# Performance work log

Hardware: AMD Instinct MI355X
Metric: run time of the kernel (lower is better)

## Reference

```python
import jax, jax.numpy as jnp
import numpy as np

CUTOFF = 10.0
EPS_W = 1e-5
EPS_LN = 1e-5

def _silu(v):
    return v * jax.nn.sigmoid(v)

def setup_inputs() -> dict:
    key = jax.random.key(0)
    ks = jax.random.split(key, 12)
    N, E, H, R = 50000, 300000, 256, 64
    s = lambda fan_in: 1.0 / np.sqrt(fan_in)
    inp = {
        'x': jax.random.normal(ks[0], (N, H), jnp.float32),
        'edge_index': jax.random.randint(ks[1], (2, E), 0, N, jnp.int64 if jax.config.jax_enable_x64 else jnp.int32),
        'distances': jax.random.uniform(ks[2], (E,), jnp.float32) * CUTOFF,
        'centers': jnp.linspace(0.0, CUTOFF, R).astype(jnp.float32),
        'widths': jnp.full((R,), CUTOFF / R, jnp.float32),
        'rbf_w1': jax.random.normal(ks[3], (R, R), jnp.float32) * s(R),
        'rbf_b1': jnp.zeros((R,), jnp.float32),
        'rbf_w2': jax.random.normal(ks[4], (R, R), jnp.float32) * s(R),
        'rbf_b2': jnp.zeros((R,), jnp.float32),
        'filt_w1': jax.random.normal(ks[5], (R, H), jnp.float32) * s(R),
        'filt_b1': jnp.zeros((H,), jnp.float32),
        'filt_w2': jax.random.normal(ks[6], (H, H), jnp.float32) * s(H),
        'filt_b2': jnp.zeros((H,), jnp.float32),
        'filt_w3': jax.random.normal(ks[7], (H, H), jnp.float32) * s(H),
        'filt_b3': jnp.zeros((H,), jnp.float32),
        'node_w': jax.random.normal(ks[8], (H, H), jnp.float32) * s(H),
        'node_b': jnp.zeros((H,), jnp.float32),
        'ln_g': jnp.ones((H,), jnp.float32),
        'ln_b': jnp.zeros((H,), jnp.float32),
        'gate_w': jax.random.normal(ks[9], (H, H), jnp.float32) * s(H),
        'gate_b': jnp.zeros((H,), jnp.float32),
    }
    return inp

def reference(x, edge_index, distances, centers, widths,
              rbf_w1, rbf_b1, rbf_w2, rbf_b2,
              filt_w1, filt_b1, filt_w2, filt_b2, filt_w3, filt_b3,
              node_w, node_b, ln_g, ln_b, gate_w, gate_b):
    # LearnableRBF: envelope * gaussian basis, then 2-layer SiLU proj
    d = distances
    env = 0.5 * (jnp.cos(d * jnp.pi / CUTOFF) + 1.0) * (d < CUTOFF).astype(x.dtype)  # [E]
    rbf = jnp.exp(-0.5 * ((d[:, None] - centers) / (jnp.abs(widths) + EPS_W)) ** 2)   # [E,R]
    r = rbf * env[:, None]
    r = _silu(r @ rbf_w1 + rbf_b1) @ rbf_w2 + rbf_b2                                  # [E,R]
    # filter network: Lin-SiLU-Lin-SiLU-Lin
    W = _silu(r @ filt_w1 + filt_b1)
    W = _silu(W @ filt_w2 + filt_b2) @ filt_w3 + filt_b3                              # [E,H]
    # gather -> modulate -> scatter-add (CFConv messaging)
    row, col = edge_index[0], edge_index[1]
    msg = (x[col] @ node_w + node_b) * W                                              # [E,H]
    agg = jax.ops.segment_sum(msg, row, num_segments=x.shape[0])                      # [N,H]
    h = x + agg
    mu = jnp.mean(h, axis=-1, keepdims=True)
    var = jnp.var(h, axis=-1, keepdims=True)
    out = (h - mu) / jnp.sqrt(var + EPS_LN) * ln_g + ln_b
    return out * jax.nn.sigmoid(out @ gate_w + gate_b)
```

## Files before the change

### kernel.cpp

```cpp
#include <hip/hip_runtime.h>
#include <hip/hip_bf16.h>
#include <math.h>

typedef __attribute__((ext_vector_type(8))) short bf16x8;
typedef __attribute__((ext_vector_type(4))) float f32x4;
typedef unsigned short ushort_t;

constexpr float F_CUTOFF = 10.0f;
constexpr float F_EPS_W  = 1e-5f;
constexpr float F_EPS_LN = 1e-5f;
constexpr float F_PI     = 3.14159265358979323846f;

__device__ __forceinline__ float silu_f(float v)   { return v / (1.0f + __expf(-v)); }
__device__ __forceinline__ float sigmoid_f(float v){ return 1.0f / (1.0f + __expf(-v)); }

__device__ __forceinline__ ushort_t f2bf(float f) {
    union { __hip_bfloat16 h; ushort_t u; } v; v.h = __float2bfloat16(f); return v.u;
}
__device__ __forceinline__ float bf2f(ushort_t u) {
    union { unsigned u; float f; } v; v.u = ((unsigned)u) << 16; return v.f;
}

__device__ __forceinline__ float f4c(const float4& v, int q) {
    return q == 0 ? v.x : q == 1 ? v.y : q == 2 ? v.z : v.w;
}

__global__ void count_kernel(const int* __restrict__ eidx, int* __restrict__ cnt, int E)
{
    int e = blockIdx.x * 256 + threadIdx.x;
    if (e < E) atomicAdd(&cnt[eidx[e]], 1);
}

__global__ __launch_bounds__(1024)
void scan_kernel(int* __restrict__ cnt ,
                 int* __restrict__ start, int N)
{
    __shared__ int part[1024];
    const int tid = threadIdx.x;
    const int C = (N + 1023) >> 10;
    const int base = tid * C;
    int s = 0;
    for (int i = 0; i < C; ++i) {
        int idx = base + i;
        if (idx < N) s += cnt[idx];
    }
    part[tid] = s;
    __syncthreads();
    for (int off = 1; off < 1024; off <<= 1) {
        int v = (tid >= off) ? part[tid - off] : 0;
        __syncthreads();
        part[tid] += v;
        __syncthreads();
    }
    int run = part[tid] - s;
    for (int i = 0; i < C; ++i) {
        int idx = base + i;
        if (idx < N) {
            int c = cnt[idx];
            start[idx] = run;
            cnt[idx]   = run;
            run += c;
        }
    }
    if (tid == 1023) start[N] = part[1023];
}

__global__ void scatter_kernel(const int* __restrict__ eidx, const float* __restrict__ dist,
                               int* __restrict__ cursor,
                               int* __restrict__ colp, int* __restrict__ nodep,
                               float* __restrict__ distp, int E)
{
    int e = blockIdx.x * 256 + threadIdx.x;
    if (e < E) {
        int row = eidx[e];
        int s = atomicAdd(&cursor[row], 1);
        colp[s]  = eidx[E + e];
        nodep[s] = row;
        distp[s] = dist[e];
    }
}

__global__ void cvt_transpose_kernel(const float* __restrict__ in, ushort_t* __restrict__ out,
                                     int K, int N, int logK)
{
    int idx = blockIdx.x * 256 + threadIdx.x;
    if (idx >= K * N) return;
    int n = idx >> logK;
    int k = idx & (K - 1);
    out[idx] = f2bf(in[k * N + n]);
}

__global__ void combine_w_kernel(const float* __restrict__ w2, const float* __restrict__ fw1,
                                 ushort_t* __restrict__ out)
{
    int idx = blockIdx.x * 256 + threadIdx.x;
    int c = idx >> 6, j = idx & 63;
    float s = 0.f;
    #pragma unroll 8
    for (int n = 0; n < 64; ++n) s += w2[j * 64 + n] * fw1[n * 256 + c];
    out[idx] = f2bf(s);
}

__global__ void combine_b_kernel(const float* __restrict__ b2, const float* __restrict__ fw1,
                                 const float* __restrict__ fb1, float* __restrict__ out)
{
    int c = threadIdx.x;
    float s = fb1[c];
    #pragma unroll 8
    for (int n = 0; n < 64; ++n) s += b2[n] * fw1[n * 256 + c];
    out[c] = s;
}

__global__ __launch_bounds__(256)
void gemm256_bf16_kernel(const float* __restrict__ A, const float* __restrict__ Wm,
                         const float* __restrict__ bias, ushort_t* __restrict__ out, int M)
{
    __shared__ float4 As4[64][64];
    const int t = threadIdx.x;
    const int row0 = blockIdx.x * 64;

    #pragma unroll
    for (int i = 0; i < 16; ++i) {
        int flat = t + i * 256;
        int r = flat >> 6, k4 = flat & 63;
        int row = row0 + r;
        float4 v = make_float4(0.f, 0.f, 0.f, 0.f);
        if (row < M) v = reinterpret_cast<const float4*>(A)[row * 64 + k4];
        As4[r][k4] = v;
    }
    __syncthreads();

    const int jt  = t & 31;
    const int et  = t >> 5;
    const int j04 = jt * 2;
    const int r0  = et * 8;

    float acc[8][8];
    #pragma unroll
    for (int r = 0; r < 8; ++r)
        #pragma unroll
        for (int c = 0; c < 8; ++c) acc[r][c] = 0.f;

    for (int k4 = 0; k4 < 64; ++k4) {
        float4 a4[8];
        #pragma unroll
        for (int r = 0; r < 8; ++r) a4[r] = As4[r0 + r][k4];
        #pragma unroll
        for (int q = 0; q < 4; ++q) {
            const int k = k4 * 4 + q;
            float4 b0 = reinterpret_cast<const float4*>(Wm)[k * 64 + j04];
            float4 b1 = reinterpret_cast<const float4*>(Wm)[k * 64 + j04 + 1];
            float bb[8] = {b0.x, b0.y, b0.z, b0.w, b1.x, b1.y, b1.z, b1.w};
            #pragma unroll
            for (int r = 0; r < 8; ++r) {
                float av = f4c(a4[r], q);
                #pragma unroll
                for (int c = 0; c < 8; ++c) acc[r][c] = fmaf(av, bb[c], acc[r][c]);
            }
        }
    }

    float4 bv0 = reinterpret_cast<const float4*>(bias)[j04];
    float4 bv1 = reinterpret_cast<const float4*>(bias)[j04 + 1];
    float bb[8] = {bv0.x, bv0.y, bv0.z, bv0.w, bv1.x, bv1.y, bv1.z, bv1.w};

    #pragma unroll
    for (int r = 0; r < 8; ++r) {
        int row = row0 + r0 + r;
        if (row >= M) continue;
        ushort_t o8[8];
        #pragma unroll
        for (int c = 0; c < 8; ++c) o8[c] = f2bf(acc[r][c] + bb[c]);
        *reinterpret_cast<uint4*>(out + (size_t)row * 256 + jt * 8) = *reinterpret_cast<uint4*>(o8);
    }
}

__global__ __launch_bounds__(256)
void gate_gemm_kernel(const float* __restrict__ A, const float* __restrict__ Wm,
                      const float* __restrict__ bias, float* __restrict__ out, int M)
{
    __shared__ float4 As4[64][64];
    const int t = threadIdx.x;
    const int row0 = blockIdx.x * 64;

    #pragma unroll
    for (int i = 0; i < 16; ++i) {
        int flat = t + i * 256;
        int r = flat >> 6, k4 = flat & 63;
        int row = row0 + r;
        float4 v = make_float4(0.f, 0.f, 0.f, 0.f);
        if (row < M) v = reinterpret_cast<const float4*>(A)[row * 64 + k4];
        As4[r][k4] = v;
    }
    __syncthreads();

    const int jt  = t & 31;
    const int et  = t >> 5;
    const int j04 = jt * 2;
    const int r0  = et * 8;

    float acc[8][8];
    #pragma unroll
    for (int r = 0; r < 8; ++r)
        #pragma unroll
        for (int c = 0; c < 8; ++c) acc[r][c] = 0.f;

    for (int k4 = 0; k4 < 64; ++k4) {
        float4 a4[8];
        #pragma unroll
        for (int r = 0; r < 8; ++r) a4[r] = As4[r0 + r][k4];
        #pragma unroll
        for (int q = 0; q < 4; ++q) {
            const int k = k4 * 4 + q;
            float4 b0 = reinterpret_cast<const float4*>(Wm)[k * 64 + j04];
            float4 b1 = reinterpret_cast<const float4*>(Wm)[k * 64 + j04 + 1];
            float bb[8] = {b0.x, b0.y, b0.z, b0.w, b1.x, b1.y, b1.z, b1.w};
            #pragma unroll
            for (int r = 0; r < 8; ++r) {
                float av = f4c(a4[r], q);
                #pragma unroll
                for (int c = 0; c < 8; ++c) acc[r][c] = fmaf(av, bb[c], acc[r][c]);
            }
        }
    }

    float4 bv0 = reinterpret_cast<const float4*>(bias)[j04];
    float4 bv1 = reinterpret_cast<const float4*>(bias)[j04 + 1];
    float bb[8] = {bv0.x, bv0.y, bv0.z, bv0.w, bv1.x, bv1.y, bv1.z, bv1.w};

    #pragma unroll
    for (int r = 0; r < 8; ++r) {
        int row = row0 + r0 + r;
        if (row >= M) continue;
        float4 a0 = As4[r0 + r][j04];
        float4 a1 = As4[r0 + r][j04 + 1];
        float aa[8] = {a0.x, a0.y, a0.z, a0.w, a1.x, a1.y, a1.z, a1.w};
        float o[8];
        #pragma unroll
        for (int c = 0; c < 8; ++c) o[c] = aa[c] * sigmoid_f(acc[r][c] + bb[c]);
        reinterpret_cast<float4*>(out)[row * 64 + j04]     = make_float4(o[0], o[1], o[2], o[3]);
        reinterpret_cast<float4*>(out)[row * 64 + j04 + 1] = make_float4(o[4], o[5], o[6], o[7]);
    }
}

template<int KS, int NT, bool SILU>
__device__ __forceinline__ void mlp_stage(const unsigned char* in, unsigned char* out,
                                          const ushort_t* __restrict__ Wt,
                                          const float* __restrict__ bias,
                                          int wn, int g, int q)
{
    constexpr int K = KS * 32;
    f32x4 acc[2][NT];
    #pragma unroll
    for (int mt = 0; mt < 2; ++mt)
        #pragma unroll
        for (int nt = 0; nt < NT; ++nt) acc[mt][nt] = (f32x4){0.f, 0.f, 0.f, 0.f};

    #pragma unroll
    for (int kk = 0; kk < KS; ++kk) {
        bf16x8 b[NT];
        #pragma unroll
        for (int nt = 0; nt < NT; ++nt) {
            int n = (wn * NT + nt) * 16 + q;
            b[nt] = *reinterpret_cast<const bf16x8*>(Wt + n * K + kk * 32 + g * 8);
        }
        bf16x8 a[2];
        #pragma unroll
        for (int mt = 0; mt < 2; ++mt) {
            int m = mt * 16 + q;
            int unit = (4 * kk + g) ^ (m & 7);
            a[mt] = *reinterpret_cast<const bf16x8*>(in + m * 512 + unit * 16);
        }
        #pragma unroll
        for (int mt = 0; mt < 2; ++mt)
            #pragma unroll
            for (int nt = 0; nt < NT; ++nt)
                acc[mt][nt] = __builtin_amdgcn_mfma_f32_16x16x32_bf16(a[mt], b[nt], acc[mt][nt], 0, 0, 0);
    }

    const bool evenq = (q & 1) == 0;
    #pragma unroll
    for (int nt = 0; nt < NT; ++nt) {
        int n0  = (wn * NT + nt) * 16 + q;
        int n_e = n0 & ~1;
        float2 bv = *reinterpret_cast<const float2*>(bias + n_e);
        #pragma unroll
        for (int mt = 0; mt < 2; ++mt) {
            float v[4], p[4];
            #pragma unroll
            for (int r = 0; r < 4; ++r) { v[r] = acc[mt][nt][r]; p[r] = __shfl_xor(v[r], 1, 64); }
            #pragma unroll
            for (int rr = 0; rr < 2; ++rr) {
                int r = evenq ? rr : (2 + rr);
                float lo = (evenq ? v[r] : p[r]) + bv.x;
                float hi = (evenq ? p[r] : v[r]) + bv.y;
                if (SILU) { lo = silu_f(lo); hi = silu_f(hi); }
                int m = mt * 16 + 4 * g + r;
                unsigned u = (unsigned)f2bf(lo) | ((unsigned)f2bf(hi) << 16);
                int byte = m * 512 + (((n_e >> 3) ^ (m & 7)) << 4) + ((n_e & 7) * 2);
                *reinterpret_cast<unsigned*>(out + byte) = u;
            }
        }
    }
}

__global__ __launch_bounds__(256, 4)
void edge_csr_kernel(const float* __restrict__ distp, const int* __restrict__ colp,
                     const int* __restrict__ nodep, const int* __restrict__ start,
                     const float* __restrict__ centers, const float* __restrict__ widths,
                     const ushort_t* __restrict__ wt_rbf1, const float* __restrict__ rbf_b1,
                     const ushort_t* __restrict__ wt_comb, const float* __restrict__ b_comb,
                     const ushort_t* __restrict__ wt_f2, const float* __restrict__ filt_b2,
                     const ushort_t* __restrict__ wt_f3, const float* __restrict__ filt_b3,
                     const ushort_t* __restrict__ y, float* __restrict__ agg, int E)
{
    __shared__ __align__(16) unsigned char buf[32768];
    __shared__ int node_s[32];
    __shared__ int flag_s[32];
    unsigned char* bufA = buf;
    unsigned char* bufB = buf + 16384;

    const int t  = threadIdx.x;
    const int e0 = blockIdx.x * 32;
    const int wn   = t >> 6;
    const int lane = t & 63;
    const int g = lane >> 4, q = lane & 15;

    if (t < 32) {
        int ge = e0 + t;
        int nd = (ge < E) ? nodep[ge] : -1;
        node_s[t] = nd;
        int fl = 0;
        if (nd >= 0) {
            int lo = start[nd], hi = start[nd + 1];
            fl = (lo >= e0 && hi <= e0 + 32) ? 1 : 0;
        }
        flag_s[t] = fl;
    }

    const int e_own  = t >> 3;
    const int chunk  = t & 7;
    const int ge_own = e0 + e_own;
    const int col_own = (ge_own < E) ? colp[ge_own] : 0;
    uint4 yv[4];
    #pragma unroll
    for (int i = 0; i < 4; ++i)
        yv[i] = *reinterpret_cast<const uint4*>(y + (size_t)col_own * 256 + (i * 8 + chunk) * 8);

    {
        float d = (ge_own < E) ? distp[ge_own] : F_CUTOFF;
        float env = (d < F_CUTOFF) ? 0.5f * (__cosf(d * (F_PI / F_CUTOFF)) + 1.0f) : 0.0f;
        unsigned char* rowp = bufA + e_own * 512;
        int k0 = chunk * 8;
        #pragma unroll
        for (int i = 0; i < 4; ++i) {
            int n = k0 + 2 * i;
            float c0 = centers[n],     w0 = fabsf(widths[n]) + F_EPS_W;
            float c1 = centers[n + 1], w1 = fabsf(widths[n + 1]) + F_EPS_W;
            float z0 = (d - c0) / w0, z1 = (d - c1) / w1;
            float r0 = env * __expf(-0.5f * z0 * z0);
            float r1 = env * __expf(-0.5f * z1 * z1);
            unsigned u = (unsigned)f2bf(r0) | ((unsigned)f2bf(r1) << 16);
            int byte = (((n >> 3) ^ (e_own & 7)) << 4) + ((n & 7) * 2);
            *reinterpret_cast<unsigned*>(rowp + byte) = u;
        }
    }
    __syncthreads();

    mlp_stage<2, 1, true>(bufA, bufB, wt_rbf1, rbf_b1, wn, g, q);
    __syncthreads();
    mlp_stage<2, 4, true>(bufB, bufA, wt_comb, b_comb, wn, g, q);
    __syncthreads();
    mlp_stage<8, 4, true>(bufA, bufB, wt_f2, filt_b2, wn, g, q);
    __syncthreads();

    #pragma unroll
    for (int i = 0; i < 4; ++i)
        *reinterpret_cast<uint4*>(bufA + e_own * 512 + (i * 8 + chunk) * 16) = yv[i];
    __syncthreads();

    f32x4 acc[2][4];
    #pragma unroll
    for (int mt = 0; mt < 2; ++mt)
        #pragma unroll
        for (int nt = 0; nt < 4; ++nt) acc[mt][nt] = (f32x4){0.f, 0.f, 0.f, 0.f};

    #pragma unroll
    for (int kk = 0; kk < 8; ++kk) {
        bf16x8 b[4];
        #pragma unroll
        for (int nt = 0; nt < 4; ++nt) {
            int n = (wn * 4 + nt) * 16 + q;
            b[nt] = *reinterpret_cast<const bf16x8*>(wt_f3 + n * 256 + kk * 32 + g * 8);
        }
        bf16x8 a[2];
        #pragma unroll
        for (int mt = 0; mt < 2; ++mt) {
            int m = mt * 16 + q;
            int unit = (4 * kk + g) ^ (m & 7);
            a[mt] = *reinterpret_cast<const bf16x8*>(bufB + m * 512 + unit * 16);
        }
        #pragma unroll
        for (int mt = 0; mt < 2; ++mt)
            #pragma unroll
            for (int nt = 0; nt < 4; ++nt)
                acc[mt][nt] = __builtin_amdgcn_mfma_f32_16x16x32_bf16(a[mt], b[nt], acc[mt][nt], 0, 0, 0);
    }

    float bn[4];
    int   nn[4];
    #pragma unroll
    for (int nt = 0; nt < 4; ++nt) { nn[nt] = (wn * 4 + nt) * 16 + q; bn[nt] = filt_b3[nn[nt]]; }

    #pragma unroll
    for (int mt = 0; mt < 2; ++mt) {
        #pragma unroll
        for (int r = 0; r < 4; ++r) {
            int m = mt * 16 + 4 * g + r;
            const unsigned char* yrow = bufA + m * 512;
            #pragma unroll
            for (int nt = 0; nt < 4; ++nt) {
                float yvv = bf2f(*reinterpret_cast<const ushort_t*>(yrow + nn[nt] * 2));
                acc[mt][nt][r] = (acc[mt][nt][r] + bn[nt]) * yvv;
            }
        }
    }
    __syncthreads();

    float* msgf = reinterpret_cast<float*>(buf);
    #pragma unroll
    for (int mt = 0; mt < 2; ++mt) {
        #pragma unroll
        for (int r = 0; r < 4; ++r) {
            int m  = mt * 16 + 4 * g + r;
            #pragma unroll
            for (int nt = 0; nt < 4; ++nt)
                msgf[m * 256 + nn[nt]] = acc[mt][nt][r];
        }
    }
    __syncthreads();

    {
        const int j = t;
        float accv = 0.f;
        int cur = -2, rs = 0;
        #pragma unroll 4
        for (int r = 0; r < 32; ++r) {
            int nd = node_s[r];
            if (nd != cur) {
                if (cur >= 0) {
                    if (flag_s[rs]) agg[(size_t)cur * 256 + j] = accv;
                    else            unsafeAtomicAdd(&agg[(size_t)cur * 256 + j], accv);
                }
                cur = nd; rs = r; accv = msgf[r * 256 + j];
            } else {
                accv += msgf[r * 256 + j];
            }
        }
        if (cur >= 0) {
            if (flag_s[rs]) agg[(size_t)cur * 256 + j] = accv;
            else            unsafeAtomicAdd(&agg[(size_t)cur * 256 + j], accv);
        }
    }
}

__global__ __launch_bounds__(256, 4)
void edge_atomic_kernel(const float* __restrict__ dist, const int* __restrict__ eidx,
                        const float* __restrict__ centers, const float* __restrict__ widths,
                        const ushort_t* __restrict__ wt_rbf1, const float* __restrict__ rbf_b1,
                        const ushort_t* __restrict__ wt_comb, const float* __restrict__ b_comb,
                        const ushort_t* __restrict__ wt_f2, const float* __restrict__ filt_b2,
                        const ushort_t* __restrict__ wt_f3, const float* __restrict__ filt_b3,
                        const ushort_t* __restrict__ y, float* __restrict__ agg, int E)
{
    __shared__ __align__(16) unsigned char bufA[16384];
    __shared__ __align__(16) unsigned char bufB[16384];
    __shared__ int rs_s[32];

    const int t  = threadIdx.x;
    const int e0 = blockIdx.x * 32;
    const int wn   = t >> 6;
    const int lane = t & 63;
    const int g = lane >> 4, q = lane & 15;

    if (t < 32) {
        int ge = e0 + t;
        rs_s[t] = (ge < E) ? eidx[ge] : 0;
    }

    const int e_own  = t >> 3;
    const int chunk  = t & 7;
    const int ge_own = e0 + e_own;
    const int col_own = (ge_own < E) ? eidx[E + ge_own] : 0;
    uint4 yv[4];
    #pragma unroll
    for (int i = 0; i < 4; ++i)
        yv[i] = *reinterpret_cast<const uint4*>(y + (size_t)col_own * 256 + (i * 8 + chunk) * 8);

    {
        float d = (ge_own < E) ? dist[ge_own] : F_CUTOFF;
        float env = (d < F_CUTOFF) ? 0.5f * (__cosf(d * (F_PI / F_CUTOFF)) + 1.0f) : 0.0f;
        unsigned char* rowp = bufA + e_own * 512;
        int k0 = chunk * 8;
        #pragma unroll
        for (int i = 0; i < 4; ++i) {
            int n = k0 + 2 * i;
            float c0 = centers[n],     w0 = fabsf(widths[n]) + F_EPS_W;
            float c1 = centers[n + 1], w1 = fabsf(widths[n + 1]) + F_EPS_W;
            float z0 = (d - c0) / w0, z1 = (d - c1) / w1;
            float r0 = env * __expf(-0.5f * z0 * z0);
            float r1 = env * __expf(-0.5f * z1 * z1);
            unsigned u = (unsigned)f2bf(r0) | ((unsigned)f2bf(r1) << 16);
            int byte = (((n >> 3) ^ (e_own & 7)) << 4) + ((n & 7) * 2);
            *reinterpret_cast<unsigned*>(rowp + byte) = u;
        }
    }
    __syncthreads();

    mlp_stage<2, 1, true>(bufA, bufB, wt_rbf1, rbf_b1, wn, g, q);
    __syncthreads();
    mlp_stage<2, 4, true>(bufB, bufA, wt_comb, b_comb, wn, g, q);
    __syncthreads();
    mlp_stage<8, 4, true>(bufA, bufB, wt_f2, filt_b2, wn, g, q);
    __syncthreads();

    #pragma unroll
    for (int i = 0; i < 4; ++i)
        *reinterpret_cast<uint4*>(bufA + e_own * 512 + (i * 8 + chunk) * 16) = yv[i];
    __syncthreads();

    {
        f32x4 acc[2][4];
        #pragma unroll
        for (int mt = 0; mt < 2; ++mt)
            #pragma unroll
            for (int nt = 0; nt < 4; ++nt) acc[mt][nt] = (f32x4){0.f, 0.f, 0.f, 0.f};

        #pragma unroll
        for (int kk = 0; kk < 8; ++kk) {
            bf16x8 b[4];
            #pragma unroll
            for (int nt = 0; nt < 4; ++nt) {
                int n = (wn * 4 + nt) * 16 + q;
                b[nt] = *reinterpret_cast<const bf16x8*>(wt_f3 + n * 256 + kk * 32 + g * 8);
            }
            bf16x8 a[2];
            #pragma unroll
            for (int mt = 0; mt < 2; ++mt) {
                int m = mt * 16 + q;
                int unit = (4 * kk + g) ^ (m & 7);
                a[mt] = *reinterpret_cast<const bf16x8*>(bufB + m * 512 + unit * 16);
            }
            #pragma unroll
            for (int mt = 0; mt < 2; ++mt)
                #pragma unroll
                for (int nt = 0; nt < 4; ++nt)
                    acc[mt][nt] = __builtin_amdgcn_mfma_f32_16x16x32_bf16(a[mt], b[nt], acc[mt][nt], 0, 0, 0);
        }

        float bn[4];
        int   nn[4];
        #pragma unroll
        for (int nt = 0; nt < 4; ++nt) { nn[nt] = (wn * 4 + nt) * 16 + q; bn[nt] = filt_b3[nn[nt]]; }

        #pragma unroll
        for (int mt = 0; mt < 2; ++mt) {
            #pragma unroll
            for (int r = 0; r < 4; ++r) {
                int m  = mt * 16 + 4 * g + r;
                int ge = e0 + m;
                if (ge < E) {
                    const unsigned char* yrow = bufA + m * 512;
                    float* arow = agg + (size_t)rs_s[m] * 256;
                    #pragma unroll
                    for (int nt = 0; nt < 4; ++nt) {
                        float wv = acc[mt][nt][r] + bn[nt];
                        float yvv = bf2f(*reinterpret_cast<const ushort_t*>(yrow + nn[nt] * 2));
                        unsafeAtomicAdd(&arow[nn[nt]], wv * yvv);
                    }
                }
            }
        }
    }
}

__global__ __launch_bounds__(256)
void ln_kernel(const float* __restrict__ x, const float* __restrict__ agg,
               const float* __restrict__ g, const float* __restrict__ b,
               float* __restrict__ out0, int N)
{
    int lane = threadIdx.x & 63;
    int row  = blockIdx.x * 4 + (threadIdx.x >> 6);
    if (row >= N) return;
    float4 hx = reinterpret_cast<const float4*>(x)[row * 64 + lane];
    float4 ha = reinterpret_cast<const float4*>(agg)[row * 64 + lane];
    float4 h  = make_float4(hx.x + ha.x, hx.y + ha.y, hx.z + ha.z, hx.w + ha.w);
    float s  = h.x + h.y + h.z + h.w;
    float s2 = h.x * h.x + h.y * h.y + h.z * h.z + h.w * h.w;
    #pragma unroll
    for (int off = 32; off > 0; off >>= 1) {
        s  += __shfl_xor(s,  off, 64);
        s2 += __shfl_xor(s2, off, 64);
    }
    float mu  = s * (1.0f / 256.0f);
    float var = s2 * (1.0f / 256.0f) - mu * mu;
    float inv = rsqrtf(var + F_EPS_LN);
    float4 gv = reinterpret_cast<const float4*>(g)[lane];
    float4 bv = reinterpret_cast<const float4*>(b)[lane];
    float4 o;
    o.x = (h.x - mu) * inv * gv.x + bv.x;
    o.y = (h.y - mu) * inv * gv.y + bv.y;
    o.z = (h.z - mu) * inv * gv.z + bv.z;
    o.w = (h.w - mu) * inv * gv.w + bv.w;
    reinterpret_cast<float4*>(out0)[row * 64 + lane] = o;
}

extern "C" void kernel_launch(void* const* d_in, const int* in_sizes, int n_in,
                              void* d_out, int out_size, void* d_ws, size_t ws_size,
                              hipStream_t stream)
{
    const float* x       = (const float*)d_in[0];
    const int*   eidx    = (const int*)  d_in[1];
    const float* dist    = (const float*)d_in[2];
    const float* centers = (const float*)d_in[3];
    const float* widths  = (const float*)d_in[4];
    const float* rbf_w1  = (const float*)d_in[5];
    const float* rbf_b1  = (const float*)d_in[6];
    const float* rbf_w2  = (const float*)d_in[7];
    const float* rbf_b2  = (const float*)d_in[8];
    const float* filt_w1 = (const float*)d_in[9];
    const float* filt_b1 = (const float*)d_in[10];
    const float* filt_w2 = (const float*)d_in[11];
    const float* filt_b2 = (const float*)d_in[12];
    const float* filt_w3 = (const float*)d_in[13];
    const float* filt_b3 = (const float*)d_in[14];
    const float* node_w  = (const float*)d_in[15];
    const float* node_b  = (const float*)d_in[16];
    const float* ln_g    = (const float*)d_in[17];
    const float* ln_b    = (const float*)d_in[18];
    const float* gate_w  = (const float*)d_in[19];
    const float* gate_b  = (const float*)d_in[20];

    const int N = in_sizes[0] / 256;
    const int E = in_sizes[2];

    char* wsb = (char*)d_ws;
    size_t off = 0;
    auto alloc = [&](size_t bytes, size_t align) -> char* {
        off = (off + align - 1) & ~(align - 1);
        char* p = wsb + off;
        off += bytes;
        return p;
    };
    ushort_t* y_bf  = (ushort_t*)alloc((size_t)N * 256 * 2, 16);
    ushort_t* wt1   = (ushort_t*)alloc(64 * 64 * 2, 16);
    ushort_t* wcomb = (ushort_t*)alloc(256 * 64 * 2, 16);
    ushort_t* wf2t  = (ushort_t*)alloc(256 * 256 * 2, 16);
    ushort_t* wf3t  = (ushort_t*)alloc(256 * 256 * 2, 16);
    float*    bcomb = (float*)   alloc(256 * 4, 16);
    int*      cnt   = (int*)     alloc((size_t)N * 4, 16);
    int*      start = (int*)     alloc(((size_t)N + 1) * 4, 16);
    int*      colp  = (int*)     alloc((size_t)E * 4, 16);
    int*      nodep = (int*)     alloc((size_t)E * 4, 16);
    float*    distp = (float*)   alloc((size_t)E * 4, 16);
    const bool csr_fits = (off <= ws_size);

    dim3 b256(256);

    cvt_transpose_kernel<<<dim3((64 * 64 + 255) / 256),   b256, 0, stream>>>(rbf_w1,  wt1, 64, 64, 6);
    combine_w_kernel<<<dim3(64), b256, 0, stream>>>(rbf_w2, filt_w1, wcomb);
    combine_b_kernel<<<dim3(1), b256, 0, stream>>>(rbf_b2, filt_w1, filt_b1, bcomb);
    cvt_transpose_kernel<<<dim3((256 * 256 + 255) / 256), b256, 0, stream>>>(filt_w2, wf2t, 256, 256, 8);
    cvt_transpose_kernel<<<dim3((256 * 256 + 255) / 256), b256, 0, stream>>>(filt_w3, wf3t, 256, 256, 8);

    gemm256_bf16_kernel<<<dim3((N + 63) / 64), b256, 0, stream>>>(x, node_w, node_b, y_bf, N);

    hipMemsetAsync(d_out, 0, (size_t)out_size * sizeof(float), stream);

    if (csr_fits) {
        hipMemsetAsync(cnt, 0, (size_t)N * 4, stream);
        count_kernel<<<dim3((E + 255) / 256), b256, 0, stream>>>(eidx, cnt, E);
        scan_kernel<<<dim3(1), 1024, 0, stream>>>(cnt, start, N);
        scatter_kernel<<<dim3((E + 255) / 256), b256, 0, stream>>>(eidx, dist, cnt, colp, nodep, distp, E);

        edge_csr_kernel<<<dim3((E + 31) / 32), b256, 0, stream>>>(
            distp, colp, nodep, start, centers, widths,
            wt1, rbf_b1, wcomb, bcomb,
            wf2t, filt_b2, wf3t, filt_b3,
            y_bf, (float*)d_out, E);
    } else {
        edge_atomic_kernel<<<dim3((E + 31) / 32), b256, 0, stream>>>(
            dist, eidx, centers, widths,
            wt1, rbf_b1, wcomb, bcomb,
            wf2t, filt_b2, wf3t, filt_b3,
            y_bf, (float*)d_out, E);
    }

    ln_kernel<<<dim3((N + 3) / 4), b256, 0, stream>>>(x, (float*)d_out, ln_g, ln_b, (float*)d_out, N);
    gate_gemm_kernel<<<dim3((N + 63) / 64), b256, 0, stream>>>((float*)d_out, gate_w, gate_b, (float*)d_out, N);
}
```

Baseline: 948.0 us.

## Split fused edge kernel into staged 64-row GEMM kernels and parallelize CSR scan

Replaces the single fused per-32-edge kernel with three kernels per edge chunk: RBF plus first filter layers written to a bf16 workspace, a double-buffered 64-row GEMM for filt_w2, and a GEMM fused with the y-gather and segmented scatter for filt_w3. The chunk size is set by the available workspace, and the split path is used only when E fits in at most 8 chunks. The aim is larger GEMM tiles with better weight reuse than 32-edge blocks provide, at the cost of extra global memory round-trips for intermediates. The single-block scan is also replaced with a two-level scan, and the atomic fallback kernel is removed.

Result: slower. 1.080 ms (+14.0%).

```diff
diff --git a/kernel.cpp b/kernel.cpp
--- a/kernel.cpp
+++ b/kernel.cpp
@@ -31,38 +31,53 @@
     if (e < E) atomicAdd(&cnt[eidx[e]], 1);
 }
 
-__global__ __launch_bounds__(1024)
-void scan_kernel(int* __restrict__ cnt ,
-                 int* __restrict__ start, int N)
-{
-    __shared__ int part[1024];
-    const int tid = threadIdx.x;
-    const int C = (N + 1023) >> 10;
-    const int base = tid * C;
+__global__ __launch_bounds__(256)
+void scan_sum_kernel(const int* __restrict__ cnt, int* __restrict__ part, int N, int range)
+{
+    __shared__ int red[256];
+    int base = blockIdx.x * range;
     int s = 0;
-    for (int i = 0; i < C; ++i) {
+    for (int i = threadIdx.x; i < range; i += 256) {
         int idx = base + i;
         if (idx < N) s += cnt[idx];
     }
-    part[tid] = s;
-    __syncthreads();
-    for (int off = 1; off < 1024; off <<= 1) {
-        int v = (tid >= off) ? part[tid - off] : 0;
+    red[threadIdx.x] = s;
+    __syncthreads();
+    #pragma unroll
+    for (int o = 128; o > 0; o >>= 1) {
+        if (threadIdx.x < o) red[threadIdx.x] += red[threadIdx.x + o];
         __syncthreads();
-        part[tid] += v;
+    }
+    if (threadIdx.x == 0) part[blockIdx.x] = red[0];
+}
+
+__global__ __launch_bounds__(256)
+void scan_write_kernel(const int* __restrict__ part, int* __restrict__ cnt ,
+                       int* __restrict__ start, int N, int range, int E)
+{
+    __shared__ int ex[256];
+    int tid = threadIdx.x;
+    int v = part[tid];
+    ex[tid] = v;
+    __syncthreads();
+    for (int o = 1; o < 256; o <<= 1) {
+        int add = (tid >= o) ? ex[tid - o] : 0;
         __syncthreads();
-    }
-    int run = part[tid] - s;
-    for (int i = 0; i < C; ++i) {
+        ex[tid] += add;
+        __syncthreads();
+    }
+    int run = ex[tid] - v;
+    int base = tid * range;
+    for (int i = 0; i < range; ++i) {
         int idx = base + i;
         if (idx < N) {
             int c = cnt[idx];
             start[idx] = run;
-            cnt[idx]   = run;
+            cnt[idx] = run;
             run += c;
         }
     }
-    if (tid == 1023) start[N] = part[1023];
+    if (tid == 0) start[N] = E;
 }
 
 __global__ void scatter_kernel(const int* __restrict__ eidx, const float* __restrict__ dist,
@@ -305,20 +320,14 @@
 }
 
 __global__ __launch_bounds__(256, 4)
-void edge_csr_kernel(const float* __restrict__ distp, const int* __restrict__ colp,
-                     const int* __restrict__ nodep, const int* __restrict__ start,
-                     const float* __restrict__ centers, const float* __restrict__ widths,
-                     const ushort_t* __restrict__ wt_rbf1, const float* __restrict__ rbf_b1,
-                     const ushort_t* __restrict__ wt_comb, const float* __restrict__ b_comb,
-                     const ushort_t* __restrict__ wt_f2, const float* __restrict__ filt_b2,
-                     const ushort_t* __restrict__ wt_f3, const float* __restrict__ filt_b3,
-                     const ushort_t* __restrict__ y, float* __restrict__ agg, int E)
-{
-    __shared__ __align__(16) unsigned char buf[32768];
-    __shared__ int node_s[32];
-    __shared__ int flag_s[32];
-    unsigned char* bufA = buf;
-    unsigned char* bufB = buf + 16384;
+void rbf_f1_kernel(const float* __restrict__ distp,
+                   const float* __restrict__ centers, const float* __restrict__ widths,
+                   const ushort_t* __restrict__ wt_rbf1, const float* __restrict__ rbf_b1,
+                   const ushort_t* __restrict__ wt_comb, const float* __restrict__ b_comb,
+                   ushort_t* __restrict__ f1, int Mc)
+{
+    __shared__ __align__(16) unsigned char bufA[16384];
+    __shared__ __align__(16) unsigned char bufB[16384];
 
     const int t  = threadIdx.x;
     const int e0 = blockIdx.x * 32;
@@ -326,29 +335,12 @@
     const int lane = t & 63;
     const int g = lane >> 4, q = lane & 15;
 
-    if (t < 32) {
-        int ge = e0 + t;
-        int nd = (ge < E) ? nodep[ge] : -1;
-        node_s[t] = nd;
-        int fl = 0;
-        if (nd >= 0) {
-            int lo = start[nd], hi = start[nd + 1];
-            fl = (lo >= e0 && hi <= e0 + 32) ? 1 : 0;
-        }
-        flag_s[t] = fl;
-    }
-
     const int e_own  = t >> 3;
     const int chunk  = t & 7;
     const int ge_own = e0 + e_own;
-    const int col_own = (ge_own < E) ? colp[ge_own] : 0;
-    uint4 yv[4];
-    #pragma unroll
-    for (int i = 0; i < 4; ++i)
-        yv[i] = *reinterpret_cast<const uint4*>(y + (size_t)col_own * 256 + (i * 8 + chunk) * 8);
 
     {
-        float d = (ge_own < E) ? distp[ge_own] : F_CUTOFF;
+        float d = (ge_own < Mc) ? distp[ge_own] : F_CUTOFF;
         float env = (d < F_CUTOFF) ? 0.5f * (__cosf(d * (F_PI / F_CUTOFF)) + 1.0f) : 0.0f;
         unsigned char* rowp = bufA + e_own * 512;
         int k0 = chunk * 8;
@@ -371,6 +363,308 @@
     __syncthreads();
     mlp_stage<2, 4, true>(bufB, bufA, wt_comb, b_comb, wn, g, q);
     __syncthreads();
+
+    if (ge_own < Mc) {
+        #pragma unroll
+        for (int i = 0; i < 4; ++i) {
+            int c = chunk + i * 8;
+            int u = (c & 24) | ((c ^ (e_own & 7)) & 7);
+            uint4 v = *reinterpret_cast<const uint4*>(bufA + e_own * 512 + u * 16);
+            *reinterpret_cast<uint4*>(f1 + (size_t)ge_own * 256 + c * 8) = v;
+        }
+    }
+}
+
+__global__ __launch_bounds__(256, 3)
+void gemm_stage_kernel(const ushort_t* __restrict__ A, const ushort_t* __restrict__ Wt,
+                       const float* __restrict__ bias, ushort_t* __restrict__ out, int M)
+{
+    __shared__ __align__(16) unsigned char sbuf[2][8192];
+
+    const int t  = threadIdx.x;
+    const int m0 = blockIdx.x * 64;
+    const int wn   = t >> 6;
+    const int lane = t & 63;
+    const int g = lane >> 4, q = lane & 15;
+
+    const int s0r = t >> 3,         s0u = t & 7;
+    const int s1r = (t + 256) >> 3, s1u = t & 7;
+    const ushort_t* src0base = A + (size_t)((m0 + s0r < M) ? (m0 + s0r) : (M - 1)) * 256 + ((s0u ^ (s0r & 7)) * 8);
+    const ushort_t* src1base = A + (size_t)((m0 + s1r < M) ? (m0 + s1r) : (M - 1)) * 256 + ((s1u ^ (s1r & 7)) * 8);
+
+    uint4 p0 = *reinterpret_cast<const uint4*>(src0base);
+    uint4 p1 = *reinterpret_cast<const uint4*>(src1base);
+    *reinterpret_cast<uint4*>(&sbuf[0][t * 16])         = p0;
+    *reinterpret_cast<uint4*>(&sbuf[0][(t + 256) * 16]) = p1;
+    __syncthreads();
+
+    f32x4 acc[4][4];
+    #pragma unroll
+    for (int mt = 0; mt < 4; ++mt)
+        #pragma unroll
+        for (int nt = 0; nt < 4; ++nt) acc[mt][nt] = (f32x4){0.f, 0.f, 0.f, 0.f};
+
+    for (int kt = 0; kt < 4; ++kt) {
+        const int cur = kt & 1;
+        uint4 nx0, nx1;
+        if (kt < 3) {
+            nx0 = *reinterpret_cast<const uint4*>(src0base + (kt + 1) * 64);
+            nx1 = *reinterpret_cast<const uint4*>(src1base + (kt + 1) * 64);
+        }
+        #pragma unroll
+        for (int ks = 0; ks < 2; ++ks) {
+            bf16x8 b[4];
+            #pragma unroll
+            for (int nt = 0; nt < 4; ++nt) {
+                int n = wn * 64 + nt * 16 + q;
+                b[nt] = *reinterpret_cast<const bf16x8*>(Wt + (size_t)n * 256 + kt * 64 + ks * 32 + g * 8);
+            }
+            bf16x8 a[4];
+            #pragma unroll
+            for (int mt = 0; mt < 4; ++mt) {
+                int r = mt * 16 + q;
+                int u = (ks * 4 + g) ^ (r & 7);
+                a[mt] = *reinterpret_cast<const bf16x8*>(&sbuf[cur][r * 128 + u * 16]);
+            }
+            #pragma unroll
+            for (int mt = 0; mt < 4; ++mt)
+                #pragma unroll
+                for (int nt = 0; nt < 4; ++nt)
+                    acc[mt][nt] = __builtin_amdgcn_mfma_f32_16x16x32_bf16(a[mt], b[nt], acc[mt][nt], 0, 0, 0);
+        }
+        __syncthreads();
+        if (kt < 3) {
+            *reinterpret_cast<uint4*>(&sbuf[cur ^ 1][t * 16])         = nx0;
+            *reinterpret_cast<uint4*>(&sbuf[cur ^ 1][(t + 256) * 16]) = nx1;
+            __syncthreads();
+        }
+    }
+
+    const bool evenq = (q & 1) == 0;
+    #pragma unroll
+    for (int nt = 0; nt < 4; ++nt) {
+        int n0  = wn * 64 + nt * 16 + q;
+        int n_e = n0 & ~1;
+        float2 bv = *reinterpret_cast<const float2*>(bias + n_e);
+        #pragma unroll
+        for (int mt = 0; mt < 4; ++mt) {
+            float v[4], p[4];
+            #pragma unroll
+            for (int r = 0; r < 4; ++r) { v[r] = acc[mt][nt][r]; p[r] = __shfl_xor(v[r], 1, 64); }
+            #pragma unroll
+            for (int rr = 0; rr < 2; ++rr) {
+                int r = evenq ? rr : (2 + rr);
+                float lo = silu_f((evenq ? v[r] : p[r]) + bv.x);
+                float hi = silu_f((evenq ? p[r] : v[r]) + bv.y);
+                int mloc = mt * 16 + 4 * g + r;
+                int grow = m0 + mloc;
+                if (grow < M) {
+                    unsigned u = (unsigned)f2bf(lo) | ((unsigned)f2bf(hi) << 16);
+                    *reinterpret_cast<unsigned*>(out + (size_t)grow * 256 + n_e) = u;
+                }
+            }
+        }
+    }
+}
+
+__global__ __launch_bounds__(256, 3)
+void gemm_scatter_kernel(const ushort_t* __restrict__ A, const ushort_t* __restrict__ Wt,
+                         const float* __restrict__ bias,
+                         const int* __restrict__ colp, const int* __restrict__ nodep,
+                         const int* __restrict__ start,
+                         const ushort_t* __restrict__ y, float* __restrict__ agg,
+                         int cs, int M)
+{
+    __shared__ __align__(16) unsigned char sbuf[2][8192];
+    __shared__ float msgf[32][257];
+    __shared__ int node_s[64], lo_s[64], hi_s[64], col_s[64];
+
+    const int t  = threadIdx.x;
+    const int m0 = blockIdx.x * 64;
+    const int gs0 = cs + m0;
+    const int wn   = t >> 6;
+    const int lane = t & 63;
+    const int g = lane >> 4, q = lane & 15;
+
+    if (t < 64) {
+        bool ok = (m0 + t < M);
+        int nd = ok ? nodep[gs0 + t] : -1;
+        node_s[t] = nd;
+        col_s[t]  = ok ? colp[gs0 + t] : 0;
+        lo_s[t] = (nd >= 0) ? start[nd] : 0;
+        hi_s[t] = (nd >= 0) ? start[nd + 1] : 0;
+    }
+
+    const int s0r = t >> 3,         s0u = t & 7;
+    const int s1r = (t + 256) >> 3, s1u = t & 7;
+    const ushort_t* src0base = A + (size_t)((m0 + s0r < M) ? (m0 + s0r) : (M - 1)) * 256 + ((s0u ^ (s0r & 7)) * 8);
+    const ushort_t* src1base = A + (size_t)((m0 + s1r < M) ? (m0 + s1r) : (M - 1)) * 256 + ((s1u ^ (s1r & 7)) * 8);
+
+    uint4 p0 = *reinterpret_cast<const uint4*>(src0base);
+    uint4 p1 = *reinterpret_cast<const uint4*>(src1base);
+    *reinterpret_cast<uint4*>(&sbuf[0][t * 16])         = p0;
+    *reinterpret_cast<uint4*>(&sbuf[0][(t + 256) * 16]) = p1;
+    __syncthreads();
+
+    f32x4 acc[4][4];
+    #pragma unroll
+    for (int mt = 0; mt < 4; ++mt)
+        #pragma unroll
+        for (int nt = 0; nt < 4; ++nt) acc[mt][nt] = (f32x4){0.f, 0.f, 0.f, 0.f};
+
+    for (int kt = 0; kt < 4; ++kt) {
+        const int cur = kt & 1;
+        uint4 nx0, nx1;
+        if (kt < 3) {
+            nx0 = *reinterpret_cast<const uint4*>(src0base + (kt + 1) * 64);
+            nx1 = *reinterpret_cast<const uint4*>(src1base + (kt + 1) * 64);
+        }
+        #pragma unroll
+        for (int ks = 0; ks < 2; ++ks) {
+            bf16x8 b[4];
+            #pragma unroll
+            for (int nt = 0; nt < 4; ++nt) {
+                int n = wn * 64 + nt * 16 + q;
+                b[nt] = *reinterpret_cast<const bf16x8*>(Wt + (size_t)n * 256 + kt * 64 + ks * 32 + g * 8);
+            }
+            bf16x8 a[4];
+            #pragma unroll
+            for (int mt = 0; mt < 4; ++mt) {
+                int r = mt * 16 + q;
+                int u = (ks * 4 + g) ^ (r & 7);
+                a[mt] = *reinterpret_cast<const bf16x8*>(&sbuf[cur][r * 128 + u * 16]);
+            }
+            #pragma unroll
+            for (int mt = 0; mt < 4; ++mt)
+                #pragma unroll
+                for (int nt = 0; nt < 4; ++nt)
+                    acc[mt][nt] = __builtin_amdgcn_mfma_f32_16x16x32_bf16(a[mt], b[nt], acc[mt][nt], 0, 0, 0);
+        }
+        __syncthreads();
+        if (kt < 3) {
+            *reinterpret_cast<uint4*>(&sbuf[cur ^ 1][t * 16])         = nx0;
+            *reinterpret_cast<uint4*>(&sbuf[cur ^ 1][(t + 256) * 16]) = nx1;
+            __syncthreads();
+        }
+    }
+
+    float bn[4];
+    #pragma unroll
+    for (int nt = 0; nt < 4; ++nt) bn[nt] = bias[wn * 64 + nt * 16 + q];
+
+    #pragma unroll
+    for (int p = 0; p < 2; ++p) {
+        #pragma unroll
+        for (int mtl = 0; mtl < 2; ++mtl) {
+            int mt = 2 * p + mtl;
+            #pragma unroll
+            for (int r = 0; r < 4; ++r) {
+                int pr = mtl * 16 + 4 * g + r;
+                #pragma unroll
+                for (int nt = 0; nt < 4; ++nt)
+                    msgf[pr][wn * 64 + nt * 16 + q] = acc[mt][nt][r] + bn[nt];
+            }
+        }
+        __syncthreads();
+
+        {
+            const int j = t;
+            const int gwin0 = gs0 + p * 32;
+            float accv = 0.f;
+            int cur = -2, curRow = 0;
+            for (int pr = 0; pr < 32; ++pr) {
+                int rr = p * 32 + pr;
+                int nd = node_s[rr];
+                float yv = bf2f(y[(size_t)col_s[rr] * 256 + j]);
+                float val = msgf[pr][j] * yv;
+                if (nd != cur) {
+                    if (cur >= 0) {
+                        bool interior = (lo_s[curRow] >= gwin0) && (hi_s[curRow] <= gwin0 + 32);
+                        if (interior) agg[(size_t)cur * 256 + j] = accv;
+                        else          unsafeAtomicAdd(&agg[(size_t)cur * 256 + j], accv);
+                    }
+                    cur = nd; curRow = rr; accv = val;
+                } else {
+                    accv += val;
+                }
+            }
+            if (cur >= 0) {
+                bool interior = (lo_s[curRow] >= gwin0) && (hi_s[curRow] <= gwin0 + 32);
+                if (interior) agg[(size_t)cur * 256 + j] = accv;
+                else          unsafeAtomicAdd(&agg[(size_t)cur * 256 + j], accv);
+            }
+        }
+        __syncthreads();
+    }
+}
+
+__global__ __launch_bounds__(256, 4)
+void edge_csr_kernel(const float* __restrict__ distp, const int* __restrict__ colp,
+                     const int* __restrict__ nodep, const int* __restrict__ start,
+                     const float* __restrict__ centers, const float* __restrict__ widths,
+                     const ushort_t* __restrict__ wt_rbf1, const float* __restrict__ rbf_b1,
+                     const ushort_t* __restrict__ wt_comb, const float* __restrict__ b_comb,
+                     const ushort_t* __restrict__ wt_f2, const float* __restrict__ filt_b2,
+                     const ushort_t* __restrict__ wt_f3, const float* __restrict__ filt_b3,
+                     const ushort_t* __restrict__ y, float* __restrict__ agg, int E)
+{
+    __shared__ __align__(16) unsigned char buf[32768];
+    __shared__ int node_s[32];
+    __shared__ int flag_s[32];
+    unsigned char* bufA = buf;
+    unsigned char* bufB = buf + 16384;
+
+    const int t  = threadIdx.x;
+    const int e0 = blockIdx.x * 32;
+    const int wn   = t >> 6;
+    const int lane = t & 63;
+    const int g = lane >> 4, q = lane & 15;
+
+    if (t < 32) {
+        int ge = e0 + t;
+        int nd = (ge < E) ? nodep[ge] : -1;
+        node_s[t] = nd;
+        int fl = 0;
+        if (nd >= 0) {
+            int lo = start[nd], hi = start[nd + 1];
+            fl = (lo >= e0 && hi <= e0 + 32) ? 1 : 0;
+        }
+        flag_s[t] = fl;
+    }
+
+    const int e_own  = t >> 3;
+    const int chunk  = t & 7;
+    const int ge_own = e0 + e_own;
+    const int col_own = (ge_own < E) ? colp[ge_own] : 0;
+    uint4 yv[4];
+    #pragma unroll
+    for (int i = 0; i < 4; ++i)
+        yv[i] = *reinterpret_cast<const uint4*>(y + (size_t)col_own * 256 + (i * 8 + chunk) * 8);
+
+    {
+        float d = (ge_own < E) ? distp[ge_own] : F_CUTOFF;
+        float env = (d < F_CUTOFF) ? 0.5f * (__cosf(d * (F_PI / F_CUTOFF)) + 1.0f) : 0.0f;
+        unsigned char* rowp = bufA + e_own * 512;
+        int k0 = chunk * 8;
+        #pragma unroll
+        for (int i = 0; i < 4; ++i) {
+            int n = k0 + 2 * i;
+            float c0 = centers[n],     w0 = fabsf(widths[n]) + F_EPS_W;
+            float c1 = centers[n + 1], w1 = fabsf(widths[n + 1]) + F_EPS_W;
+            float z0 = (d - c0) / w0, z1 = (d - c1) / w1;
+            float r0 = env * __expf(-0.5f * z0 * z0);
+            float r1 = env * __expf(-0.5f * z1 * z1);
+            unsigned u = (unsigned)f2bf(r0) | ((unsigned)f2bf(r1) << 16);
+            int byte = (((n >> 3) ^ (e_own & 7)) << 4) + ((n & 7) * 2);
+            *reinterpret_cast<unsigned*>(rowp + byte) = u;
+        }
+    }
+    __syncthreads();
+
+    mlp_stage<2, 1, true>(bufA, bufB, wt_rbf1, rbf_b1, wn, g, q);
+    __syncthreads();
+    mlp_stage<2, 4, true>(bufB, bufA, wt_comb, b_comb, wn, g, q);
+    __syncthreads();
     mlp_stage<8, 4, true>(bufA, bufB, wt_f2, filt_b2, wn, g, q);
     __syncthreads();
 
@@ -432,7 +726,7 @@
     for (int mt = 0; mt < 2; ++mt) {
         #pragma unroll
         for (int r = 0; r < 4; ++r) {
-            int m  = mt * 16 + 4 * g + r;
+            int m = mt * 16 + 4 * g + r;
             #pragma unroll
             for (int nt = 0; nt < 4; ++nt)
                 msgf[m * 256 + nn[nt]] = acc[mt][nt][r];
@@ -460,126 +754,6 @@
         if (cur >= 0) {
             if (flag_s[rs]) agg[(size_t)cur * 256 + j] = accv;
             else            unsafeAtomicAdd(&agg[(size_t)cur * 256 + j], accv);
-        }
-    }
-}
-
-__global__ __launch_bounds__(256, 4)
-void edge_atomic_kernel(const float* __restrict__ dist, const int* __restrict__ eidx,
-                        const float* __restrict__ centers, const float* __restrict__ widths,
-                        const ushort_t* __restrict__ wt_rbf1, const float* __restrict__ rbf_b1,
-                        const ushort_t* __restrict__ wt_comb, const float* __restrict__ b_comb,
-                        const ushort_t* __restrict__ wt_f2, const float* __restrict__ filt_b2,
-                        const ushort_t* __restrict__ wt_f3, const float* __restrict__ filt_b3,
-                        const ushort_t* __restrict__ y, float* __restrict__ agg, int E)
-{
-    __shared__ __align__(16) unsigned char bufA[16384];
-    __shared__ __align__(16) unsigned char bufB[16384];
-    __shared__ int rs_s[32];
-
-    const int t  = threadIdx.x;
-    const int e0 = blockIdx.x * 32;
-    const int wn   = t >> 6;
-    const int lane = t & 63;
-    const int g = lane >> 4, q = lane & 15;
-
-    if (t < 32) {
-        int ge = e0 + t;
-        rs_s[t] = (ge < E) ? eidx[ge] : 0;
-    }
-
-    const int e_own  = t >> 3;
-    const int chunk  = t & 7;
-    const int ge_own = e0 + e_own;
-    const int col_own = (ge_own < E) ? eidx[E + ge_own] : 0;
-    uint4 yv[4];
-    #pragma unroll
-    for (int i = 0; i < 4; ++i)
-        yv[i] = *reinterpret_cast<const uint4*>(y + (size_t)col_own * 256 + (i * 8 + chunk) * 8);
-
-    {
-        float d = (ge_own < E) ? dist[ge_own] : F_CUTOFF;
-        float env = (d < F_CUTOFF) ? 0.5f * (__cosf(d * (F_PI / F_CUTOFF)) + 1.0f) : 0.0f;
-        unsigned char* rowp = bufA + e_own * 512;
-        int k0 = chunk * 8;
-        #pragma unroll
-        for (int i = 0; i < 4; ++i) {
-            int n = k0 + 2 * i;
-            float c0 = centers[n],     w0 = fabsf(widths[n]) + F_EPS_W;
-            float c1 = centers[n + 1], w1 = fabsf(widths[n + 1]) + F_EPS_W;
-            float z0 = (d - c0) / w0, z1 = (d - c1) / w1;
-            float r0 = env * __expf(-0.5f * z0 * z0);
-            float r1 = env * __expf(-0.5f * z1 * z1);
-            unsigned u = (unsigned)f2bf(r0) | ((unsigned)f2bf(r1) << 16);
-            int byte = (((n >> 3) ^ (e_own & 7)) << 4) + ((n & 7) * 2);
-            *reinterpret_cast<unsigned*>(rowp + byte) = u;
-        }
-    }
-    __syncthreads();
-
-    mlp_stage<2, 1, true>(bufA, bufB, wt_rbf1, rbf_b1, wn, g, q);
-    __syncthreads();
-    mlp_stage<2, 4, true>(bufB, bufA, wt_comb, b_comb, wn, g, q);
-    __syncthreads();
-    mlp_stage<8, 4, true>(bufA, bufB, wt_f2, filt_b2, wn, g, q);
-    __syncthreads();
-
-    #pragma unroll
-    for (int i = 0; i < 4; ++i)
-        *reinterpret_cast<uint4*>(bufA + e_own * 512 + (i * 8 + chunk) * 16) = yv[i];
-    __syncthreads();
-
-    {
-        f32x4 acc[2][4];
-        #pragma unroll
-        for (int mt = 0; mt < 2; ++mt)
-            #pragma unroll
-            for (int nt = 0; nt < 4; ++nt) acc[mt][nt] = (f32x4){0.f, 0.f, 0.f, 0.f};
-
-        #pragma unroll
-        for (int kk = 0; kk < 8; ++kk) {
-            bf16x8 b[4];
-            #pragma unroll
-            for (int nt = 0; nt < 4; ++nt) {
-                int n = (wn * 4 + nt) * 16 + q;
-                b[nt] = *reinterpret_cast<const bf16x8*>(wt_f3 + n * 256 + kk * 32 + g * 8);
-            }
-            bf16x8 a[2];
-            #pragma unroll
-            for (int mt = 0; mt < 2; ++mt) {
-                int m = mt * 16 + q;
-                int unit = (4 * kk + g) ^ (m & 7);
-                a[mt] = *reinterpret_cast<const bf16x8*>(bufB + m * 512 + unit * 16);
-            }
-            #pragma unroll
-            for (int mt = 0; mt < 2; ++mt)
-                #pragma unroll
-                for (int nt = 0; nt < 4; ++nt)
-                    acc[mt][nt] = __builtin_amdgcn_mfma_f32_16x16x32_bf16(a[mt], b[nt], acc[mt][nt], 0, 0, 0);
-        }
-
-        float bn[4];
-        int   nn[4];
-        #pragma unroll
-        for (int nt = 0; nt < 4; ++nt) { nn[nt] = (wn * 4 + nt) * 16 + q; bn[nt] = filt_b3[nn[nt]]; }
-
-        #pragma unroll
-        for (int mt = 0; mt < 2; ++mt) {
-            #pragma unroll
-            for (int r = 0; r < 4; ++r) {
-                int m  = mt * 16 + 4 * g + r;
-                int ge = e0 + m;
-                if (ge < E) {
-                    const unsigned char* yrow = bufA + m * 512;
-                    float* arow = agg + (size_t)rs_s[m] * 256;
-                    #pragma unroll
-                    for (int nt = 0; nt < 4; ++nt) {
-                        float wv = acc[mt][nt][r] + bn[nt];
-                        float yvv = bf2f(*reinterpret_cast<const ushort_t*>(yrow + nn[nt] * 2));
-                        unsafeAtomicAdd(&arow[nn[nt]], wv * yvv);
-                    }
-                }
-            }
         }
     }
 }
@@ -658,14 +832,25 @@
     ushort_t* wf2t  = (ushort_t*)alloc(256 * 256 * 2, 16);
     ushort_t* wf3t  = (ushort_t*)alloc(256 * 256 * 2, 16);
     float*    bcomb = (float*)   alloc(256 * 4, 16);
+    int*      part  = (int*)     alloc(256 * 4, 16);
     int*      cnt   = (int*)     alloc((size_t)N * 4, 16);
     int*      start = (int*)     alloc(((size_t)N + 1) * 4, 16);
     int*      colp  = (int*)     alloc((size_t)E * 4, 16);
     int*      nodep = (int*)     alloc((size_t)E * 4, 16);
-    float*    distp = (float*)   alloc((size_t)E * 4, 16);
-    const bool csr_fits = (off <= ws_size);
+    float*    distp = (float*)   alloc((size_t)E * 4, 256);
+
+    size_t fixed_off = (off + 1023) & ~(size_t)1023;
+    size_t avail = (ws_size > fixed_off) ? (ws_size - fixed_off) : 0;
+    long Rl = (long)(avail / 1024);
+    int R = (int)(Rl & ~63L);
+    int Eround = (E + 63) & ~63;
+    if (R > Eround) R = Eround;
+    const bool dense = (R >= 64) && ((E + R - 1) / R <= 8);
+    ushort_t* f1 = (ushort_t*)(wsb + fixed_off);
+    ushort_t* f2 = f1 + (size_t)R * 256;
 
     dim3 b256(256);
+    const int range = (N + 255) / 256;
 
     cvt_transpose_kernel<<<dim3((64 * 64 + 255) / 256),   b256, 0, stream>>>(rbf_w1,  wt1, 64, 64, 6);
     combine_w_kernel<<<dim3(64), b256, 0, stream>>>(rbf_w2, filt_w1, wcomb);
@@ -676,24 +861,29 @@
     gemm256_bf16_kernel<<<dim3((N + 63) / 64), b256, 0, stream>>>(x, node_w, node_b, y_bf, N);
 
     hipMemsetAsync(d_out, 0, (size_t)out_size * sizeof(float), stream);
-
-    if (csr_fits) {
-        hipMemsetAsync(cnt, 0, (size_t)N * 4, stream);
-        count_kernel<<<dim3((E + 255) / 256), b256, 0, stream>>>(eidx, cnt, E);
-        scan_kernel<<<dim3(1), 1024, 0, stream>>>(cnt, start, N);
-        scatter_kernel<<<dim3((E + 255) / 256), b256, 0, stream>>>(eidx, dist, cnt, colp, nodep, distp, E);
-
+    hipMemsetAsync(cnt, 0, (size_t)N * 4, stream);
+
+    count_kernel<<<dim3((E + 255) / 256), b256, 0, stream>>>(eidx, cnt, E);
+    scan_sum_kernel<<<dim3(256), b256, 0, stream>>>(cnt, part, N, range);
+    scan_write_kernel<<<dim3(1), b256, 0, stream>>>(part, cnt, start, N, range, E);
+    scatter_kernel<<<dim3((E + 255) / 256), b256, 0, stream>>>(eidx, dist, cnt, colp, nodep, distp, E);
+
+    if (dense) {
+        for (int cs = 0; cs < E; cs += R) {
+            int Mc = (E - cs < R) ? (E - cs) : R;
+            rbf_f1_kernel<<<dim3((Mc + 31) / 32), b256, 0, stream>>>(
+                distp + cs, centers, widths, wt1, rbf_b1, wcomb, bcomb, f1, Mc);
+            gemm_stage_kernel<<<dim3((Mc + 63) / 64), b256, 0, stream>>>(
+                f1, wf2t, filt_b2, f2, Mc);
+            gemm_scatter_kernel<<<dim3((Mc + 63) / 64), b256, 0, stream>>>(
+                f2, wf3t, filt_b3, colp, nodep, start, y_bf, (float*)d_out, cs, Mc);
+        }
+    } else {
         edge_csr_kernel<<<dim3((E + 31) / 32), b256, 0, stream>>>(
             distp, colp, nodep, start, centers, widths,
             wt1, rbf_b1, wcomb, bcomb,
             wf2t, filt_b2, wf3t, filt_b3,
             y_bf, (float*)d_out, E);
-    } else {
-        edge_atomic_kernel<<<dim3((E + 31) / 32), b256, 0, stream>>>(
-            dist, eidx, centers, widths,
-            wt1, rbf_b1, wcomb, bcomb,
-            wf2t, filt_b2, wf3t, filt_b3,
-            y_bf, (float*)d_out, E);
     }
 
     ln_kernel<<<dim3((N + 3) / 4), b256, 0, stream>>>(x, (float*)d_out, ln_g, ln_b, (float*)d_out, N);
```
